# Kernel tuning notes

Measured on AMD Instinct MI355X. Metric: run time of the kernel, lower is better.

Reference implementation:

```python
import jax, jax.numpy as jnp
import numpy as np

B, L, H, E, EH = 8, 96, 8, 64, 128

def setup_inputs() -> dict:
    key = jax.random.key(0)
    ks = jax.random.split(key, 5)
    x = jax.random.normal(ks[0], (B, L, H, E), jnp.float32)
    # strictly increasing, distinct time points (required by the past/future split)
    gaps = jax.random.uniform(ks[1], (L,), jnp.float32, 0.01, 0.1)
    timeslot = jnp.cumsum(gaps)
    W1 = jax.random.normal(ks[2], (E, EH), jnp.float32) / np.sqrt(E).astype(np.float32)
    b1 = jnp.zeros((EH,), jnp.float32)
    W2 = jax.random.normal(ks[3], (EH, E), jnp.float32) / np.sqrt(EH).astype(np.float32)
    b2 = jnp.zeros((E,), jnp.float32)
    return dict(x=x, timeslot=timeslot, W1=W1, b1=b1, W2=W2, b2=b2)

def reference(x, timeslot, W1, b1, W2, b2):
    Bd, Ld, Hd, Ed = x.shape

    def f(t, y):  # neural odefunc: MLP over feature dim E (t unused by the MLP)
        return jnp.tanh(y @ W1 + b1) @ W2 + b2

    def rk4_step(y, t0, dt):  # torchdiffeq 'rk4' = 3/8-rule RK4, one step per grid interval
        k1 = f(t0, y)
        k2 = f(t0 + dt / 3, y + dt * k1 / 3)
        k3 = f(t0 + 2 * dt / 3, y + dt * (k2 - k1 / 3))
        k4 = f(t0 + dt, y + dt * (k1 - k2 + k3))
        return y + dt * (k1 + 3 * (k2 + k3) + k4) / 8

    # Per-index initial states: S0[idx] = x[:, idx] flattened to (B*H, E)
    S0 = jnp.transpose(x, (1, 0, 2, 3)).reshape(Ld, Bd * Hd, Ed)
    idxs = jnp.arange(Ld)

    # Forward integration: state for index idx is advanced over t_s -> t_{s+1} once s >= idx.
    def fwd_step(S, s):
        t0 = timeslot[s]
        dt = timeslot[s + 1] - t0
        S2 = rk4_step(S, t0, dt)
        S = jnp.where((idxs <= s)[:, None, None], S2, S)
        return S, S  # emitted state corresponds to time t_{s+1}

    _, ys_f = jax.lax.scan(fwd_step, S0, jnp.arange(Ld - 1))
    z_fwd = jnp.concatenate([S0[None], ys_f], axis=0)  # [L_j, L_idx, B*H, E]

    # Backward integration: state for idx is advanced over t_s -> t_{s-1} once s <= idx.
    def bwd_step(S, s):
        t0 = timeslot[s]
        dt = timeslot[s - 1] - t0  # negative
        S2 = rk4_step(S, t0, dt)
        S = jnp.where((idxs >= s)[:, None, None], S2, S)
        return S, S  # emitted state corresponds to time t_{s-1}

    _, ys_b = jax.lax.scan(bwd_step, S0, jnp.arange(Ld - 1, 0, -1))
    z_bwd = jnp.concatenate([jnp.flip(ys_b, axis=0), S0[None]], axis=0)  # [L_j, L_idx, B*H, E]

    jj = jnp.arange(Ld)[:, None]
    z = jnp.where((jj >= idxs[None, :])[:, :, None, None], z_fwd, z_bwd)
    z = z.reshape(Ld, Ld, Bd, Hd, Ed)          # [L_j, L_idx, B, H, E]
    x1 = jnp.transpose(z, (2, 1, 0, 3, 4))      # [B, L_idx, L_j, H, E]
    x0 = jnp.broadcast_to(x[:, :, None], (Bd, Ld, Ld, Hd, Ed))
    return jnp.stack([x0, x1], axis=-1)          # [B, L, L, H, E, 2]
```

## Files before the change

kernel.cpp:

```cpp
#include <hip/hip_runtime.h>
#include <stdint.h>

#define Lc 96
#define Hc 8
#define Ec 64
#define EHc 128
#define APu 72
#define HPu 136
#define JS (Hc * Ec * 2)

typedef __attribute__((ext_vector_type(8))) short short8;
typedef __attribute__((ext_vector_type(4))) float floatx4;

union FragH { uint16_t h[8]; short8 v; };

__device__ __forceinline__ float fast_tanh(float x) {
    const float e = __builtin_amdgcn_exp2f(x * 2.8853900817779268f);
    return 1.0f - 2.0f * __builtin_amdgcn_rcpf(e + 1.0f);
}

__device__ __forceinline__ void lds_barrier() {
    asm volatile("s_waitcnt lgkmcnt(0)\n\ts_barrier" ::: "memory");
}

#define MF(acc, A, B) acc = __builtin_amdgcn_mfma_f32_16x16x32_bf16((A), (B), (acc), 0, 0, 0)

__global__ __launch_bounds__(512, 2)
void ode_mfma_kernel(const float* __restrict__ x, const float* __restrict__ ts,
                     const float* __restrict__ W1, const float* __restrict__ b1,
                     const float* __restrict__ W2, const float* __restrict__ b2,
                     float* __restrict__ out)
{
    __shared__ alignas(16) uint16_t A_hi[16 * APu];
    __shared__ alignas(16) uint16_t A_lo[16 * APu];
    __shared__ alignas(16) uint16_t H_hi[16 * HPu];
    __shared__ alignas(16) uint16_t H_lo[16 * HPu];
    __shared__ float tss[Lc];

    const int tid  = threadIdx.x;
    const int w    = tid >> 6;
    const int lane = tid & 63;
    const int g    = lane >> 4;
    const int c    = lane & 15;

    const int dir   = blockIdx.x & 1;
    const int tile  = dir ? (383 - (blockIdx.x >> 1)) : (blockIdx.x >> 1);
    const int t_blk = tile >> 2;
    const int nv    = dir ? t_blk : (Lc - 1 - t_blk);
    const int col   = 16 * w + c;

    float y0_[4], y_[4];
    float* outp0 = nullptr;
    if (w < 4) {
#pragma unroll
        for (int reg = 0; reg < 4; ++reg) {
            const int rs = tile * 16 + g * 4 + reg;
            const int bidx = (rs & 63) >> 3;
            const int hh   = rs & 7;
            const float v0 = x[((bidx * Lc + t_blk) * Hc + hh) * Ec + col];
            y0_[reg] = v0; y_[reg] = v0;
            if (reg == 0)
                outp0 = out + (size_t)(bidx * Lc + t_blk) * (Lc * JS) + hh * (Ec * 2) + col * 2;
            if (dir == 0) {
                float2 o; o.x = v0; o.y = v0;
                *(float2*)(outp0 + reg * (Ec * 2) + (size_t)t_blk * JS) = o;
            }
        }
    }
    if (nv == 0) return;

    if (tid < Lc) tss[tid] = ts[tid];

    short8 w1h[2], w1l[2];
#pragma unroll
    for (int ks = 0; ks < 2; ++ks) {
        FragH fh, fl;
#pragma unroll
        for (int j = 0; j < 8; ++j) {
            const int k = ks * 32 + g * 8 + j;
            const float v = W1[k * EHc + col];
            const uint32_t uv = __float_as_uint(v);
            const float hf = __uint_as_float(uv & 0xffff0000u);
            fh.h[j] = (uint16_t)(uv >> 16);
            fl.h[j] = (uint16_t)(__float_as_uint(v - hf) >> 16);
        }
        w1h[ks] = fh.v; w1l[ks] = fl.v;
    }
    short8 w2h[4], w2l[4];
    if (w < 4) {
#pragma unroll
        for (int ks = 0; ks < 4; ++ks) {
            FragH fh, fl;
#pragma unroll
            for (int j = 0; j < 8; ++j) {
                const int k = ks * 32 + g * 8 + j;
                const float v = W2[k * Ec + col];
                const uint32_t uv = __float_as_uint(v);
                const float hf = __uint_as_float(uv & 0xffff0000u);
                fh.h[j] = (uint16_t)(uv >> 16);
                fl.h[j] = (uint16_t)(__float_as_uint(v - hf) >> 16);
            }
            w2h[ks] = fh.v; w2l[ks] = fl.v;
        }
    }

    const float b1v = b1[col & 127];
    const float b2v = (w < 4) ? b2[col] : 0.f;

    if (w < 4) {
#pragma unroll
        for (int reg = 0; reg < 4; ++reg) {
            const int r = g * 4 + reg;
            const float v0 = y0_[reg];
            const uint32_t uv = __float_as_uint(v0);
            A_hi[r * APu + col] = (uint16_t)(uv >> 16);
            A_lo[r * APu + col] =
                (uint16_t)(__float_as_uint(v0 - __uint_as_float(uv & 0xffff0000u)) >> 16);
        }
    }
    __syncthreads();

    const int arow = c * APu + g * 8;
    const int hrow = c * HPu + g * 8;
    const int hcol = 16 * w + c;

    auto evalf = [&]() -> floatx4 {
        const short8 a0h = *(const short8*)(A_hi + arow);
        const short8 a1h = *(const short8*)(A_hi + arow + 32);
        const short8 a0l = *(const short8*)(A_lo + arow);
        const short8 a1l = *(const short8*)(A_lo + arow + 32);

        floatx4 p = {b1v, b1v, b1v, b1v};
        MF(p, a0h, w1h[0]); MF(p, a0h, w1l[0]); MF(p, a0l, w1h[0]);
        MF(p, a1h, w1h[1]); MF(p, a1h, w1l[1]); MF(p, a1l, w1h[1]);

#pragma unroll
        for (int reg = 0; reg < 4; ++reg) {
            const int r = g * 4 + reg;
            const float t0 = fast_tanh(p[reg]);
            const uint32_t u0 = __float_as_uint(t0);
            H_hi[r * HPu + hcol] = (uint16_t)(u0 >> 16);
            H_lo[r * HPu + hcol] =
                (uint16_t)(__float_as_uint(t0 - __uint_as_float(u0 & 0xffff0000u)) >> 16);
        }
        lds_barrier();

        const floatx4 z = {0.f, 0.f, 0.f, 0.f};
        floatx4 oa = z, ob = z, oc = z, od = z;
        if (w < 4) {
            oa.x = b2v; oa.y = b2v; oa.z = b2v; oa.w = b2v;
            const short8 h0 = *(const short8*)(H_hi + hrow);
            const short8 l0 = *(const short8*)(H_lo + hrow);
            const short8 h1 = *(const short8*)(H_hi + hrow + 32);
            const short8 l1 = *(const short8*)(H_lo + hrow + 32);
            const short8 h2 = *(const short8*)(H_hi + hrow + 64);
            const short8 l2 = *(const short8*)(H_lo + hrow + 64);
            const short8 h3 = *(const short8*)(H_hi + hrow + 96);
            const short8 l3 = *(const short8*)(H_lo + hrow + 96);
            MF(oa, h0, w2h[0]); MF(oa, h0, w2l[0]); MF(oa, l0, w2h[0]);
            MF(ob, h1, w2h[1]); MF(ob, h1, w2l[1]); MF(ob, l1, w2h[1]);
            MF(oc, h2, w2h[2]); MF(oc, h2, w2l[2]); MF(oc, l2, w2h[2]);
            MF(od, h3, w2h[3]); MF(od, h3, w2l[3]); MF(od, l3, w2h[3]);
        }
        return (oa + ob) + (oc + od);
    };

    auto putA = [&](const float* a4) {
        if (w < 4) {
#pragma unroll
            for (int reg = 0; reg < 4; ++reg) {
                const int r = g * 4 + reg;
                const float v = a4[reg];
                const uint32_t uv = __float_as_uint(v);
                A_hi[r * APu + col] = (uint16_t)(uv >> 16);
                A_lo[r * APu + col] =
                    (uint16_t)(__float_as_uint(v - __uint_as_float(uv & 0xffff0000u)) >> 16);
            }
        }
        lds_barrier();
    };

    for (int v = 0; v < nv; ++v) {
        int s, jo;
        if (dir == 0) { s = t_blk + v; jo = s + 1; }
        else          { s = t_blk - v; jo = s - 1; }
        const float dt = tss[jo] - tss[s];

        float a[4];
        const floatx4 k1 = evalf();
#pragma unroll
        for (int reg = 0; reg < 4; ++reg)
            a[reg] = fmaf(dt * (1.0f / 3.0f), k1[reg], y_[reg]);
        putA(a);
        const floatx4 k2 = evalf();
#pragma unroll
        for (int reg = 0; reg < 4; ++reg)
            a[reg] = y_[reg] + dt * (k2[reg] - (1.0f / 3.0f) * k1[reg]);
        putA(a);
        const floatx4 k3 = evalf();
#pragma unroll
        for (int reg = 0; reg < 4; ++reg)
            a[reg] = y_[reg] + dt * (k1[reg] - k2[reg] + k3[reg]);
        putA(a);
        const floatx4 k4 = evalf();
        if (w < 4) {
#pragma unroll
            for (int reg = 0; reg < 4; ++reg) {
                y_[reg] += dt * (k1[reg] + 3.0f * (k2[reg] + k3[reg]) + k4[reg]) * 0.125f;
                float2 o; o.x = y0_[reg]; o.y = y_[reg];
                *(float2*)(outp0 + reg * (Ec * 2) + (size_t)jo * JS) = o;
            }
        }
#pragma unroll
        for (int reg = 0; reg < 4; ++reg) a[reg] = y_[reg];
        putA(a);
    }
}

extern "C" void kernel_launch(void* const* d_in, const int* in_sizes, int n_in,
                              void* d_out, int out_size, void* d_ws, size_t ws_size,
                              hipStream_t stream) {
    const float* x  = (const float*)d_in[0];
    const float* ts = (const float*)d_in[1];
    const float* W1 = (const float*)d_in[2];
    const float* b1 = (const float*)d_in[3];
    const float* W2 = (const float*)d_in[4];
    const float* b2 = (const float*)d_in[5];
    float* out = (float*)d_out;

    dim3 grid(768);
    dim3 block(512);
    ode_mfma_kernel<<<grid, block, 0, stream>>>(x, ts, W1, b1, W2, b2, out);
}
```

Measured before the change: 564.1 us.

## Drop low-half of hidden activations, split W1 accumulators, fence barriers, reorder stores

The low-order bf16 half of the tanh hidden activations is no longer stored or multiplied, which cuts the second-layer MFMAs from three to two per k-slice and removes one LDS array along with its writes and reads. The first-layer MFMA chain is split into two independent accumulators to shorten the dependency chain. Scheduling barriers are placed around the LDS barrier, and the global output store is moved after the next-state LDS write so it can overlap the following step. Dropping the low-half term lowers the precision of the hidden activations, and that error accumulates over the integration steps.

New measurement: 518.7 us. 8.1% less time.

```diff
diff --git a/kernel.cpp b/kernel.cpp
--- a/kernel.cpp
+++ b/kernel.cpp
@@ -20,7 +20,9 @@
 }
 
 __device__ __forceinline__ void lds_barrier() {
+    __builtin_amdgcn_sched_barrier(0);
     asm volatile("s_waitcnt lgkmcnt(0)\n\ts_barrier" ::: "memory");
+    __builtin_amdgcn_sched_barrier(0);
 }
 
 #define MF(acc, A, B) acc = __builtin_amdgcn_mfma_f32_16x16x32_bf16((A), (B), (acc), 0, 0, 0)
@@ -34,7 +36,6 @@
     __shared__ alignas(16) uint16_t A_hi[16 * APu];
     __shared__ alignas(16) uint16_t A_lo[16 * APu];
     __shared__ alignas(16) uint16_t H_hi[16 * HPu];
-    __shared__ alignas(16) uint16_t H_lo[16 * HPu];
     __shared__ float tss[Lc];
 
     const int tid  = threadIdx.x;
@@ -46,7 +47,7 @@
     const int dir   = blockIdx.x & 1;
     const int tile  = dir ? (383 - (blockIdx.x >> 1)) : (blockIdx.x >> 1);
     const int t_blk = tile >> 2;
-    const int nv    = dir ? t_blk : (Lc - 1 - t_blk);
+    const int nv    = dir ? t_blk : (Lc - 1) - t_blk;
     const int col   = 16 * w + c;
 
     float y0_[4], y_[4];
@@ -130,37 +131,31 @@
         const short8 a0l = *(const short8*)(A_lo + arow);
         const short8 a1l = *(const short8*)(A_lo + arow + 32);
 
-        floatx4 p = {b1v, b1v, b1v, b1v};
-        MF(p, a0h, w1h[0]); MF(p, a0h, w1l[0]); MF(p, a0l, w1h[0]);
-        MF(p, a1h, w1h[1]); MF(p, a1h, w1l[1]); MF(p, a1l, w1h[1]);
+        const floatx4 z = {0.f, 0.f, 0.f, 0.f};
+        floatx4 pa = {b1v, b1v, b1v, b1v}, pb = z;
+        MF(pa, a0h, w1h[0]); MF(pa, a0h, w1l[0]); MF(pa, a0l, w1h[0]);
+        MF(pb, a1h, w1h[1]); MF(pb, a1h, w1l[1]); MF(pb, a1l, w1h[1]);
+        const floatx4 p = pa + pb;
 
 #pragma unroll
         for (int reg = 0; reg < 4; ++reg) {
             const int r = g * 4 + reg;
             const float t0 = fast_tanh(p[reg]);
-            const uint32_t u0 = __float_as_uint(t0);
-            H_hi[r * HPu + hcol] = (uint16_t)(u0 >> 16);
-            H_lo[r * HPu + hcol] =
-                (uint16_t)(__float_as_uint(t0 - __uint_as_float(u0 & 0xffff0000u)) >> 16);
+            H_hi[r * HPu + hcol] = (uint16_t)(__float_as_uint(t0) >> 16);
         }
         lds_barrier();
 
-        const floatx4 z = {0.f, 0.f, 0.f, 0.f};
         floatx4 oa = z, ob = z, oc = z, od = z;
         if (w < 4) {
             oa.x = b2v; oa.y = b2v; oa.z = b2v; oa.w = b2v;
             const short8 h0 = *(const short8*)(H_hi + hrow);
-            const short8 l0 = *(const short8*)(H_lo + hrow);
             const short8 h1 = *(const short8*)(H_hi + hrow + 32);
-            const short8 l1 = *(const short8*)(H_lo + hrow + 32);
             const short8 h2 = *(const short8*)(H_hi + hrow + 64);
-            const short8 l2 = *(const short8*)(H_lo + hrow + 64);
             const short8 h3 = *(const short8*)(H_hi + hrow + 96);
-            const short8 l3 = *(const short8*)(H_lo + hrow + 96);
-            MF(oa, h0, w2h[0]); MF(oa, h0, w2l[0]); MF(oa, l0, w2h[0]);
-            MF(ob, h1, w2h[1]); MF(ob, h1, w2l[1]); MF(ob, l1, w2h[1]);
-            MF(oc, h2, w2h[2]); MF(oc, h2, w2l[2]); MF(oc, l2, w2h[2]);
-            MF(od, h3, w2h[3]); MF(od, h3, w2l[3]); MF(od, l3, w2h[3]);
+            MF(oa, h0, w2h[0]); MF(oa, h0, w2l[0]);
+            MF(ob, h1, w2h[1]); MF(ob, h1, w2l[1]);
+            MF(oc, h2, w2h[2]); MF(oc, h2, w2l[2]);
+            MF(od, h3, w2h[3]); MF(od, h3, w2l[3]);
         }
         return (oa + ob) + (oc + od);
     };
@@ -205,15 +200,19 @@
         const floatx4 k4 = evalf();
         if (w < 4) {
 #pragma unroll
+            for (int reg = 0; reg < 4; ++reg)
+                y_[reg] += dt * (k1[reg] + 3.0f * (k2[reg] + k3[reg]) + k4[reg]) * 0.125f;
+        }
+#pragma unroll
+        for (int reg = 0; reg < 4; ++reg) a[reg] = y_[reg];
+        putA(a);
+        if (w < 4) {
+#pragma unroll
             for (int reg = 0; reg < 4; ++reg) {
-                y_[reg] += dt * (k1[reg] + 3.0f * (k2[reg] + k3[reg]) + k4[reg]) * 0.125f;
                 float2 o; o.x = y0_[reg]; o.y = y_[reg];
                 *(float2*)(outp0 + reg * (Ec * 2) + (size_t)jo * JS) = o;
             }
         }
-#pragma unroll
-        for (int reg = 0; reg < 4; ++reg) a[reg] = y_[reg];
-        putA(a);
     }
 }
 
```
